# Kernel tuning notes

Hardware: AMD Instinct MI355X
Metric: run time of the kernel (lower is better)

## Reference

```python
import jax, jax.numpy as jnp
import numpy as np

WINDOW_SIZE = 64
SHIFT_SIZE = WINDOW_SIZE // 2  # shift_windows=True
HEAD_DIM = 64
SCALE = HEAD_DIM ** (-0.5)


def _shift_mask(W):
    # static shift-window mask, computed with numpy (all shapes static)
    img_mask = np.zeros((W,), dtype=np.float32)
    cnt = 0
    for s in (slice(0, -WINDOW_SIZE), slice(-WINDOW_SIZE, -SHIFT_SIZE), slice(-SHIFT_SIZE, None)):
        img_mask[s] = cnt
        cnt += 1
    mw = img_mask.reshape(W // WINDOW_SIZE, WINDOW_SIZE)  # (num_win, ws)
    mask = mw[:, None, :] - mw[:, :, None]                # (num_win, ws, ws)
    mask = np.where(mask != 0.0, -100.0, 0.0).astype(np.float32)
    return jnp.asarray(mask)


def setup_inputs() -> dict:
    key = jax.random.key(0)
    k1, k2, k3, k4 = jax.random.split(key, 4)
    B, W, C = 32, 8192, HEAD_DIM
    return {
        "q": jax.random.normal(k1, (B, W, C), dtype=jnp.float32),
        "k": jax.random.normal(k2, (B, W, C), dtype=jnp.float32),
        "v": jax.random.normal(k3, (B, W, C), dtype=jnp.float32),
        "rel_pos_table": jax.random.normal(k4, (2 * WINDOW_SIZE - 1, 1), dtype=jnp.float32) * 0.02,
    }


def reference(q, k, v, rel_pos_table):
    B, W, C = q.shape
    ws = WINDOW_SIZE
    # relative position bias gather: (1, ws, ws)
    coords = jnp.arange(ws)
    rel_idx = coords[None, :] * 0 + (coords[:, None] - coords[None, :]) + (ws - 1)  # (ws, ws)
    bias = rel_pos_table[rel_idx.reshape(-1)].reshape(ws, ws, -1)
    bias = jnp.transpose(bias, (2, 0, 1))  # (1, ws, ws)

    mask = _shift_mask(W)  # (num_win, ws, ws)

    # cyclic shift
    q = jnp.roll(q, shift=-SHIFT_SIZE, axis=1)
    k = jnp.roll(k, shift=-SHIFT_SIZE, axis=1)
    v = jnp.roll(v, shift=-SHIFT_SIZE, axis=1)

    # window partition -> (B * num_win, ws, C)
    num_win = W // ws
    qw = q.reshape(B * num_win, ws, C)
    kw = k.reshape(B * num_win, ws, C)
    vw = v.reshape(B * num_win, ws, C)

    attn = jnp.einsum('bnc,bmc->bnm', qw, kw) * SCALE + bias  # (B*nw, ws, ws)
    attn = attn.reshape(B, num_win, ws, ws) + mask[None]
    attn = attn.reshape(-1, ws, ws)
    attn = jax.nn.softmax(attn, axis=-1)

    xw = jnp.einsum('bnm,bmc->bnc', attn, vw)  # (B*nw, ws, C)
    x = xw.reshape(B, W, C)
    x = jnp.roll(x, shift=SHIFT_SIZE, axis=1)
    return (x, attn)
```

## Files before the change

### kernel.cpp

```cpp
#include <hip/hip_runtime.h>
#include <cstdint>
#include <cstddef>

#define WS 64
#define SHIFT 32
#define WTOT 8192
#define NWIN 128
#define SCALE_F 0.125f
#define LSTR 72

typedef __bf16 bf16x8 __attribute__((ext_vector_type(8)));
typedef unsigned short u16x8 __attribute__((ext_vector_type(8)));
typedef float f32x4 __attribute__((ext_vector_type(4)));

__device__ __forceinline__ void split1(float f, unsigned short& h, unsigned short& l) {
  const unsigned u = __builtin_bit_cast(unsigned, f);
  h = (unsigned short)(u >> 16);
  const float hf = __builtin_bit_cast(float, u & 0xFFFF0000u);
  const float r = f - hf;
  l = (unsigned short)(__builtin_bit_cast(unsigned, r) >> 16);
}

__device__ __forceinline__ void split8(const float* f, bf16x8& hi, bf16x8& lo) {
  u16x8 hv, lv;
#pragma unroll
  for (int e = 0; e < 8; ++e) {
    unsigned short hh, ll;
    split1(f[e], hh, ll);
    hv[e] = hh; lv[e] = ll;
  }
  hi = __builtin_bit_cast(bf16x8, hv);
  lo = __builtin_bit_cast(bf16x8, lv);
}

__device__ __forceinline__ unsigned short rne1(float f) {
  unsigned u = __builtin_bit_cast(unsigned, f);
  u += 0x7FFFu + ((u >> 16) & 1u);
  return (unsigned short)(u >> 16);
}

__global__ __launch_bounds__(256, 5) void win_attn(
    const float* __restrict__ q, const float* __restrict__ k,
    const float* __restrict__ v, const float* __restrict__ table,
    float* __restrict__ xout, float* __restrict__ attn_out) {
  __shared__ __align__(16) unsigned short s_k[2][WS * LSTR];
  __shared__ __align__(16) unsigned short s_vt[WS * LSTR];
  __shared__ float s_bias[2 * WS - 1];

  const int t = threadIdx.x;
  const int b = blockIdx.x;
  const int batch = b >> 7;
  const int win = b & (NWIN - 1);

  const int lane = t & 63;
  const int wave = t >> 6;
  const int lrow = lane & 15;
  const int quad = lane >> 4;

  const int qrow = wave * 16 + lrow;
  const int gq = (win * WS + qrow + SHIFT) & (WTOT - 1);
  const float* qp = q + ((size_t)batch * WTOT + gq) * WS;

  const int lr = t >> 2;
  const int gk = (win * WS + lr + SHIFT) & (WTOT - 1);
  const size_t gbase = ((size_t)batch * WTOT + gk) * WS;
  const int lck = (t & 3) << 4;
  const float* kp = k + gbase + lck;
  const int cv = (t & 3) << 2;
  const float* vp = v + gbase;

  float4 L[12];
  L[0] = *(const float4*)(qp + quad * 8);
  L[1] = *(const float4*)(qp + quad * 8 + 4);
  L[2] = *(const float4*)(qp + 32 + quad * 8);
  L[3] = *(const float4*)(qp + 32 + quad * 8 + 4);
  L[4] = *(const float4*)(kp + 0);
  L[5] = *(const float4*)(kp + 4);
  L[6] = *(const float4*)(kp + 8);
  L[7] = *(const float4*)(kp + 12);
  L[8]  = *(const float4*)(vp + cv);
  L[9]  = *(const float4*)(vp + cv + 16);
  L[10] = *(const float4*)(vp + cv + 32);
  L[11] = *(const float4*)(vp + cv + 48);

  if (t < 2 * WS - 1) s_bias[t] = table[t];

#pragma unroll
  for (int g = 0; g < 2; ++g) {
    const float4 f0 = L[4 + 2 * g];
    const float4 f1 = L[5 + 2 * g];
    const float fa[8] = {f0.x, f0.y, f0.z, f0.w, f1.x, f1.y, f1.z, f1.w};
    bf16x8 hi, lo;
    split8(fa, hi, lo);
    *(bf16x8*)(&s_k[0][lr * LSTR + lck + g * 8]) = hi;
    *(bf16x8*)(&s_k[1][lr * LSTR + lck + g * 8]) = lo;
  }

#pragma unroll
  for (int blk = 0; blk < 4; ++blk) {
    const float4 vv = L[8 + blk];
    const float va[4] = {vv.x, vv.y, vv.z, vv.w};
#pragma unroll
    for (int e = 0; e < 4; ++e) {
      const int cc = cv + blk * 16 + e;
      s_vt[cc * LSTR + lr] = rne1(va[e]);
    }
  }

  bf16x8 aq_hi[2], aq_lo[2];
#pragma unroll
  for (int kh = 0; kh < 2; ++kh) {
    const float4 f0 = L[2 * kh];
    const float4 f1 = L[2 * kh + 1];
    const float fa[8] = {f0.x, f0.y, f0.z, f0.w, f1.x, f1.y, f1.z, f1.w};
    split8(fa, aq_hi[kh], aq_lo[kh]);
  }
  __syncthreads();

  const f32x4 z4 = {0.f, 0.f, 0.f, 0.f};
  f32x4 acc[4] = {z4, z4, z4, z4};
#pragma unroll
  for (int kh = 0; kh < 2; ++kh) {
    const bf16x8 ahi = aq_hi[kh];
    const bf16x8 alo = aq_lo[kh];
    const int k0 = kh * 32 + quad * 8;
#pragma unroll
    for (int j = 0; j < 4; ++j) {
      const bf16x8 bhi = *(const bf16x8*)(&s_k[0][(j * 16 + lrow) * LSTR + k0]);
      const bf16x8 blo = *(const bf16x8*)(&s_k[1][(j * 16 + lrow) * LSTR + k0]);
      acc[j] = __builtin_amdgcn_mfma_f32_16x16x32_bf16(ahi, bhi, acc[j], 0, 0, 0);
      acc[j] = __builtin_amdgcn_mfma_f32_16x16x32_bf16(alo, bhi, acc[j], 0, 0, 0);
      acc[j] = __builtin_amdgcn_mfma_f32_16x16x32_bf16(ahi, blo, acc[j], 0, 0, 0);
    }
  }

  const bool masked = (win == NWIN - 1);
  float p[4][4];
#pragma unroll
  for (int reg = 0; reg < 4; ++reg) {
    const int r = wave * 16 + quad * 4 + reg;
    float val[4];
    float vmax = -1e30f;
#pragma unroll
    for (int j = 0; j < 4; ++j) {
      const int m = j * 16 + lrow;
      float s = acc[j][reg] * SCALE_F + s_bias[r - m + (WS - 1)];
      if (masked && (((r ^ m) & 32) != 0)) s -= 100.0f;
      val[j] = s;
      vmax = fmaxf(vmax, s);
    }
#pragma unroll
    for (int off = 1; off < 16; off <<= 1)
      vmax = fmaxf(vmax, __shfl_xor(vmax, off, 64));
    float sum = 0.f;
#pragma unroll
    for (int j = 0; j < 4; ++j) {
      val[j] = __expf(val[j] - vmax);
      sum += val[j];
    }
#pragma unroll
    for (int off = 1; off < 16; off <<= 1)
      sum += __shfl_xor(sum, off, 64);
    const float inv = 1.0f / sum;
#pragma unroll
    for (int j = 0; j < 4; ++j) p[reg][j] = val[j] * inv;
  }

  {
    float* arow = attn_out + (size_t)b * (WS * WS);
#pragma unroll
    for (int reg = 0; reg < 4; ++reg) {
      const int r = wave * 16 + quad * 4 + reg;
#pragma unroll
      for (int j = 0; j < 4; ++j) {
        __builtin_nontemporal_store(p[reg][j], arow + r * WS + j * 16 + lrow);
      }
    }
  }

  __syncthreads();

#pragma unroll
  for (int reg = 0; reg < 4; ++reg) {
    const int r = wave * 16 + quad * 4 + reg;
#pragma unroll
    for (int j = 0; j < 4; ++j) {
      s_k[0][r * LSTR + j * 16 + lrow] = rne1(p[reg][j]);
    }
  }

  f32x4 xacc[4] = {z4, z4, z4, z4};
#pragma unroll
  for (int kh = 0; kh < 2; ++kh) {
    const int k0 = kh * 32 + quad * 8;
    const bf16x8 phi = *(const bf16x8*)(&s_k[0][(wave * 16 + lrow) * LSTR + k0]);
#pragma unroll
    for (int j = 0; j < 4; ++j) {
      const bf16x8 vhi = *(const bf16x8*)(&s_vt[(j * 16 + lrow) * LSTR + k0]);
      xacc[j] = __builtin_amdgcn_mfma_f32_16x16x32_bf16(phi, vhi, xacc[j], 0, 0, 0);
    }
  }

#pragma unroll
  for (int reg = 0; reg < 4; ++reg) {
    const int r = wave * 16 + quad * 4 + reg;
    const int gr = (win * WS + r + SHIFT) & (WTOT - 1);
    float* xrow = xout + ((size_t)batch * WTOT + gr) * WS;
#pragma unroll
    for (int j = 0; j < 4; ++j) {
      __builtin_nontemporal_store(xacc[j][reg], xrow + j * 16 + lrow);
    }
  }
}

extern "C" void kernel_launch(void* const* d_in, const int* in_sizes, int n_in,
                              void* d_out, int out_size, void* d_ws, size_t ws_size,
                              hipStream_t stream) {
  (void)in_sizes; (void)n_in; (void)out_size; (void)d_ws; (void)ws_size;
  const float* q = (const float*)d_in[0];
  const float* k = (const float*)d_in[1];
  const float* v = (const float*)d_in[2];
  const float* table = (const float*)d_in[3];
  float* xout = (float*)d_out;
  float* attn = (float*)d_out + (size_t)32 * WTOT * WS;
  win_attn<<<dim3(4096), dim3(256), 0, stream>>>(q, k, v, table, xout, attn);
}
```

Before: 284.4 us.

## Make blocks loop over eight windows with register-prefetched loads and LDS-staged stores

```diff
diff --git a/kernel.cpp b/kernel.cpp
--- a/kernel.cpp
+++ b/kernel.cpp
@@ -8,9 +8,12 @@
 #define NWIN 128
 #define SCALE_F 0.125f
 #define LSTR 72
+#define WPB 8
+#define NBLK 512
 
 typedef __bf16 bf16x8 __attribute__((ext_vector_type(8)));
 typedef unsigned short u16x8 __attribute__((ext_vector_type(8)));
+typedef unsigned short u16x4 __attribute__((ext_vector_type(4)));
 typedef float f32x4 __attribute__((ext_vector_type(4)));
 
 __device__ __forceinline__ void split1(float f, unsigned short& h, unsigned short& l) {
@@ -38,8 +41,15 @@
   u += 0x7FFFu + ((u >> 16) & 1u);
   return (unsigned short)(u >> 16);
 }
-
-__global__ __launch_bounds__(256, 5) void win_attn(
+__device__ __forceinline__ float bf2f(unsigned short h) {
+  return __builtin_bit_cast(float, ((unsigned)h) << 16);
+}
+
+__device__ __forceinline__ void lds_barrier() {
+  asm volatile("s_waitcnt lgkmcnt(0)\n\ts_barrier" ::: "memory");
+}
+
+__global__ __launch_bounds__(256, 2) void win_attn(
     const float* __restrict__ q, const float* __restrict__ k,
     const float* __restrict__ v, const float* __restrict__ table,
     float* __restrict__ xout, float* __restrict__ attn_out) {
@@ -48,168 +58,176 @@
   __shared__ float s_bias[2 * WS - 1];
 
   const int t = threadIdx.x;
-  const int b = blockIdx.x;
-  const int batch = b >> 7;
-  const int win = b & (NWIN - 1);
-
   const int lane = t & 63;
   const int wave = t >> 6;
   const int lrow = lane & 15;
   const int quad = lane >> 4;
-
-  const int qrow = wave * 16 + lrow;
-  const int gq = (win * WS + qrow + SHIFT) & (WTOT - 1);
-  const float* qp = q + ((size_t)batch * WTOT + gq) * WS;
-
-  const int lr = t >> 2;
-  const int gk = (win * WS + lr + SHIFT) & (WTOT - 1);
-  const size_t gbase = ((size_t)batch * WTOT + gk) * WS;
-  const int lck = (t & 3) << 4;
-  const float* kp = k + gbase + lck;
-  const int cv = (t & 3) << 2;
-  const float* vp = v + gbase;
-
-  float4 L[12];
-  L[0] = *(const float4*)(qp + quad * 8);
-  L[1] = *(const float4*)(qp + quad * 8 + 4);
-  L[2] = *(const float4*)(qp + 32 + quad * 8);
-  L[3] = *(const float4*)(qp + 32 + quad * 8 + 4);
-  L[4] = *(const float4*)(kp + 0);
-  L[5] = *(const float4*)(kp + 4);
-  L[6] = *(const float4*)(kp + 8);
-  L[7] = *(const float4*)(kp + 12);
-  L[8]  = *(const float4*)(vp + cv);
-  L[9]  = *(const float4*)(vp + cv + 16);
-  L[10] = *(const float4*)(vp + cv + 32);
-  L[11] = *(const float4*)(vp + cv + 48);
+  const int srow = t >> 4;
+  const int scol = (t & 15) << 2;
 
   if (t < 2 * WS - 1) s_bias[t] = table[t];
 
-#pragma unroll
-  for (int g = 0; g < 2; ++g) {
-    const float4 f0 = L[4 + 2 * g];
-    const float4 f1 = L[5 + 2 * g];
-    const float fa[8] = {f0.x, f0.y, f0.z, f0.w, f1.x, f1.y, f1.z, f1.w};
-    bf16x8 hi, lo;
-    split8(fa, hi, lo);
-    *(bf16x8*)(&s_k[0][lr * LSTR + lck + g * 8]) = hi;
-    *(bf16x8*)(&s_k[1][lr * LSTR + lck + g * 8]) = lo;
-  }
-
-#pragma unroll
-  for (int blk = 0; blk < 4; ++blk) {
-    const float4 vv = L[8 + blk];
-    const float va[4] = {vv.x, vv.y, vv.z, vv.w};
-#pragma unroll
-    for (int e = 0; e < 4; ++e) {
-      const int cc = cv + blk * 16 + e;
-      s_vt[cc * LSTR + lr] = rne1(va[e]);
-    }
-  }
-
-  bf16x8 aq_hi[2], aq_lo[2];
-#pragma unroll
-  for (int kh = 0; kh < 2; ++kh) {
-    const float4 f0 = L[2 * kh];
-    const float4 f1 = L[2 * kh + 1];
-    const float fa[8] = {f0.x, f0.y, f0.z, f0.w, f1.x, f1.y, f1.z, f1.w};
-    split8(fa, aq_hi[kh], aq_lo[kh]);
-  }
-  __syncthreads();
-
-  const f32x4 z4 = {0.f, 0.f, 0.f, 0.f};
-  f32x4 acc[4] = {z4, z4, z4, z4};
-#pragma unroll
-  for (int kh = 0; kh < 2; ++kh) {
-    const bf16x8 ahi = aq_hi[kh];
-    const bf16x8 alo = aq_lo[kh];
-    const int k0 = kh * 32 + quad * 8;
-#pragma unroll
-    for (int j = 0; j < 4; ++j) {
-      const bf16x8 bhi = *(const bf16x8*)(&s_k[0][(j * 16 + lrow) * LSTR + k0]);
-      const bf16x8 blo = *(const bf16x8*)(&s_k[1][(j * 16 + lrow) * LSTR + k0]);
-      acc[j] = __builtin_amdgcn_mfma_f32_16x16x32_bf16(ahi, bhi, acc[j], 0, 0, 0);
-      acc[j] = __builtin_amdgcn_mfma_f32_16x16x32_bf16(alo, bhi, acc[j], 0, 0, 0);
-      acc[j] = __builtin_amdgcn_mfma_f32_16x16x32_bf16(ahi, blo, acc[j], 0, 0, 0);
-    }
-  }
-
-  const bool masked = (win == NWIN - 1);
-  float p[4][4];
-#pragma unroll
-  for (int reg = 0; reg < 4; ++reg) {
-    const int r = wave * 16 + quad * 4 + reg;
-    float val[4];
-    float vmax = -1e30f;
-#pragma unroll
-    for (int j = 0; j < 4; ++j) {
-      const int m = j * 16 + lrow;
-      float s = acc[j][reg] * SCALE_F + s_bias[r - m + (WS - 1)];
-      if (masked && (((r ^ m) & 32) != 0)) s -= 100.0f;
-      val[j] = s;
-      vmax = fmaxf(vmax, s);
-    }
-#pragma unroll
-    for (int off = 1; off < 16; off <<= 1)
-      vmax = fmaxf(vmax, __shfl_xor(vmax, off, 64));
-    float sum = 0.f;
-#pragma unroll
-    for (int j = 0; j < 4; ++j) {
-      val[j] = __expf(val[j] - vmax);
-      sum += val[j];
-    }
-#pragma unroll
-    for (int off = 1; off < 16; off <<= 1)
-      sum += __shfl_xor(sum, off, 64);
-    const float inv = 1.0f / sum;
-#pragma unroll
-    for (int j = 0; j < 4; ++j) p[reg][j] = val[j] * inv;
-  }
-
-  {
-    float* arow = attn_out + (size_t)b * (WS * WS);
+  auto issue = [&](int idx, float4* L) {
+    const int batch = idx >> 7;
+    const int win = idx & (NWIN - 1);
+    const size_t tb = (size_t)batch * WTOT;
+    const int gq = (win * WS + wave * 16 + lrow + SHIFT) & (WTOT - 1);
+    const float* qp = q + (tb + gq) * WS + quad * 8;
+    L[0] = *(const float4*)(qp);
+    L[1] = *(const float4*)(qp + 4);
+    L[2] = *(const float4*)(qp + 32);
+    L[3] = *(const float4*)(qp + 36);
+#pragma unroll
+    for (int c = 0; c < 4; ++c) {
+      const int row = c * 16 + srow;
+      const int gr = (win * WS + row + SHIFT) & (WTOT - 1);
+      const size_t base = (tb + gr) * WS + scol;
+      L[4 + c] = *(const float4*)(k + base);
+      L[8 + c] = *(const float4*)(v + base);
+    }
+  };
+
+  auto process = [&](int idx, const float4* L) {
+    const int batch = idx >> 7;
+    const int win = idx & (NWIN - 1);
+    const bool masked = (win == NWIN - 1);
+
+#pragma unroll
+    for (int c = 0; c < 4; ++c) {
+      const int row = c * 16 + srow;
+      const float4 kf = L[4 + c];
+      const float ka[4] = {kf.x, kf.y, kf.z, kf.w};
+      u16x4 h4, l4;
+#pragma unroll
+      for (int e = 0; e < 4; ++e) {
+        unsigned short h, l;
+        split1(ka[e], h, l);
+        h4[e] = h; l4[e] = l;
+      }
+      *(u16x4*)(&s_k[0][row * LSTR + scol]) = h4;
+      *(u16x4*)(&s_k[1][row * LSTR + scol]) = l4;
+      const float4 vf = L[8 + c];
+      const float va[4] = {vf.x, vf.y, vf.z, vf.w};
+#pragma unroll
+      for (int e = 0; e < 4; ++e)
+        s_vt[(scol + e) * LSTR + row] = rne1(va[e]);
+    }
+    bf16x8 aq_hi[2], aq_lo[2];
+#pragma unroll
+    for (int kh = 0; kh < 2; ++kh) {
+      const float4 f0 = L[2 * kh], f1 = L[2 * kh + 1];
+      const float fa[8] = {f0.x, f0.y, f0.z, f0.w, f1.x, f1.y, f1.z, f1.w};
+      split8(fa, aq_hi[kh], aq_lo[kh]);
+    }
+    lds_barrier();
+
+    const f32x4 z4 = {0.f, 0.f, 0.f, 0.f};
+    f32x4 acc[4] = {z4, z4, z4, z4};
+#pragma unroll
+    for (int kh = 0; kh < 2; ++kh) {
+      const int k0 = kh * 32 + quad * 8;
+#pragma unroll
+      for (int j = 0; j < 4; ++j) {
+        const bf16x8 bhi = *(const bf16x8*)(&s_k[0][(j * 16 + lrow) * LSTR + k0]);
+        const bf16x8 blo = *(const bf16x8*)(&s_k[1][(j * 16 + lrow) * LSTR + k0]);
+        acc[j] = __builtin_amdgcn_mfma_f32_16x16x32_bf16(aq_hi[kh], bhi, acc[j], 0, 0, 0);
+        acc[j] = __builtin_amdgcn_mfma_f32_16x16x32_bf16(aq_lo[kh], bhi, acc[j], 0, 0, 0);
+        acc[j] = __builtin_amdgcn_mfma_f32_16x16x32_bf16(aq_hi[kh], blo, acc[j], 0, 0, 0);
+      }
+    }
+
+    float p[4][4];
 #pragma unroll
     for (int reg = 0; reg < 4; ++reg) {
       const int r = wave * 16 + quad * 4 + reg;
-#pragma unroll
-      for (int j = 0; j < 4; ++j) {
-        __builtin_nontemporal_store(p[reg][j], arow + r * WS + j * 16 + lrow);
-      }
-    }
-  }
-
-  __syncthreads();
-
-#pragma unroll
-  for (int reg = 0; reg < 4; ++reg) {
-    const int r = wave * 16 + quad * 4 + reg;
-#pragma unroll
-    for (int j = 0; j < 4; ++j) {
-      s_k[0][r * LSTR + j * 16 + lrow] = rne1(p[reg][j]);
-    }
-  }
-
-  f32x4 xacc[4] = {z4, z4, z4, z4};
-#pragma unroll
-  for (int kh = 0; kh < 2; ++kh) {
-    const int k0 = kh * 32 + quad * 8;
-    const bf16x8 phi = *(const bf16x8*)(&s_k[0][(wave * 16 + lrow) * LSTR + k0]);
-#pragma unroll
-    for (int j = 0; j < 4; ++j) {
-      const bf16x8 vhi = *(const bf16x8*)(&s_vt[(j * 16 + lrow) * LSTR + k0]);
-      xacc[j] = __builtin_amdgcn_mfma_f32_16x16x32_bf16(phi, vhi, xacc[j], 0, 0, 0);
-    }
-  }
-
-#pragma unroll
-  for (int reg = 0; reg < 4; ++reg) {
-    const int r = wave * 16 + quad * 4 + reg;
-    const int gr = (win * WS + r + SHIFT) & (WTOT - 1);
-    float* xrow = xout + ((size_t)batch * WTOT + gr) * WS;
-#pragma unroll
-    for (int j = 0; j < 4; ++j) {
-      __builtin_nontemporal_store(xacc[j][reg], xrow + j * 16 + lrow);
-    }
+      float val[4];
+      float vmax = -1e30f;
+#pragma unroll
+      for (int j = 0; j < 4; ++j) {
+        const int m = j * 16 + lrow;
+        float s = acc[j][reg] * SCALE_F + s_bias[r - m + (WS - 1)];
+        if (masked && (((r ^ m) & 32) != 0)) s -= 100.0f;
+        val[j] = s;
+        vmax = fmaxf(vmax, s);
+      }
+#pragma unroll
+      for (int off = 1; off < 16; off <<= 1)
+        vmax = fmaxf(vmax, __shfl_xor(vmax, off, 64));
+      float sum = 0.f;
+#pragma unroll
+      for (int j = 0; j < 4; ++j) {
+        val[j] = __expf(val[j] - vmax);
+        sum += val[j];
+      }
+#pragma unroll
+      for (int off = 1; off < 16; off <<= 1)
+        sum += __shfl_xor(sum, off, 64);
+      const float inv = 1.0f / sum;
+#pragma unroll
+      for (int j = 0; j < 4; ++j) p[reg][j] = val[j] * inv;
+    }
+    lds_barrier();
+
+#pragma unroll
+    for (int reg = 0; reg < 4; ++reg) {
+      const int r = wave * 16 + quad * 4 + reg;
+#pragma unroll
+      for (int j = 0; j < 4; ++j)
+        s_k[0][r * LSTR + j * 16 + lrow] = rne1(p[reg][j]);
+    }
+
+    f32x4 xacc[4] = {z4, z4, z4, z4};
+#pragma unroll
+    for (int kh = 0; kh < 2; ++kh) {
+      const int k0 = kh * 32 + quad * 8;
+      const bf16x8 phi = *(const bf16x8*)(&s_k[0][(wave * 16 + lrow) * LSTR + k0]);
+#pragma unroll
+      for (int j = 0; j < 4; ++j) {
+        const bf16x8 vhi = *(const bf16x8*)(&s_vt[(j * 16 + lrow) * LSTR + k0]);
+        xacc[j] = __builtin_amdgcn_mfma_f32_16x16x32_bf16(phi, vhi, xacc[j], 0, 0, 0);
+      }
+    }
+    lds_barrier();
+
+    float* aw = attn_out + (size_t)idx * (WS * WS);
+#pragma unroll
+    for (int c = 0; c < 4; ++c) {
+      const int row = c * 16 + srow;
+      const u16x4 pb = *(const u16x4*)(&s_k[0][row * LSTR + scol]);
+      f32x4 o = {bf2f(pb[0]), bf2f(pb[1]), bf2f(pb[2]), bf2f(pb[3])};
+      __builtin_nontemporal_store(o, (f32x4*)(aw + (size_t)c * 1024 + t * 4));
+    }
+    lds_barrier();
+
+    float* s_xf = (float*)&s_k[0][0];
+#pragma unroll
+    for (int reg = 0; reg < 4; ++reg) {
+      const int r = wave * 16 + quad * 4 + reg;
+#pragma unroll
+      for (int j = 0; j < 4; ++j)
+        s_xf[r * 68 + j * 16 + lrow] = xacc[j][reg];
+    }
+    lds_barrier();
+#pragma unroll
+    for (int c = 0; c < 4; ++c) {
+      const int row = c * 16 + srow;
+      const f32x4 xv = *(const f32x4*)(&s_xf[row * 68 + scol]);
+      const int gr = (win * WS + row + SHIFT) & (WTOT - 1);
+      __builtin_nontemporal_store(
+          xv, (f32x4*)(xout + ((size_t)batch * WTOT + gr) * WS + scol));
+    }
+    lds_barrier();
+  };
+
+  const int idx0 = blockIdx.x * WPB;
+  float4 A[12], B[12];
+  issue(idx0, A);
+#pragma unroll 1
+  for (int i = 0; i < WPB; i += 2) {
+    issue(idx0 + i + 1, B);
+    process(idx0 + i, A);
+    if (i < WPB - 2) issue(idx0 + i + 2, A);
+    process(idx0 + i + 1, B);
   }
 }
 
@@ -223,5 +241,5 @@
   const float* table = (const float*)d_in[3];
   float* xout = (float*)d_out;
   float* attn = (float*)d_out + (size_t)32 * WTOT * WS;
-  win_attn<<<dim3(4096), dim3(256), 0, stream>>>(q, k, v, table, xout, attn);
-}
+  win_attn<<<dim3(NBLK), dim3(256), 0, stream>>>(q, k, v, table, xout, attn);
+}
```

After: 294.5 us. 3.5% more time.
